# Optimization experiments

Hardware: AMD Instinct MI355X
Metric: run time of the kernel (lower is better)

The kernel has to match this reference:

```python
import jax, jax.numpy as jnp
import numpy as np
from jax import lax

EPS = 1e-8

def _conv(x, w, b):
    # x: [B,Cin,H,W], w: [Cout,Cin,kh,kw] (torch OIHW layout), SAME padding, stride 1
    y = lax.conv_general_dilated(x, w, (1, 1), 'SAME',
                                 dimension_numbers=('NCHW', 'OIHW', 'NCHW'))
    return y + b[None, :, None, None]

def setup_inputs() -> dict:
    key = jax.random.key(0)
    ks = jax.random.split(key, 16)
    B, S, H, A, NZ, NO = 256, 4, 32, 5, 150, 17
    d = {
        'map_in': jax.random.uniform(ks[0], (B, 2, H, H), jnp.float32),
        'b0': jax.random.uniform(ks[1], (B, H, H), jnp.float32),
        'act_in': jax.random.randint(ks[2], (B, S), 0, A),
        'obs_in': jax.random.uniform(ks[3], (B, S, 4), jnp.float32),
        'is_start': 1,
        'step_size': S,
        'VI_k': 64,
        # parameters, initialized per the torch init scheme
        'Tb_w': 1.0 / 9.0 + jax.random.normal(ks[4], (A, 1, 3, 3)) / 90.0,
        'Tb_b': jnp.zeros((A,)),
        'Tv_w': 1.0 / 9.0 + jax.random.normal(ks[5], (A, 1, 3, 3)) / 90.0,
        'Tv_b': jnp.zeros((A,)),
        'Z1_w': jax.random.normal(ks[6], (NZ, 1, 3, 3)) / 3.0,
        'Z1_b': jnp.zeros((NZ,)),
        'Z2_w': jax.random.normal(ks[7], (NO, NZ, 1, 1)) / np.sqrt(NZ),
        'Z2_b': jnp.zeros((NO,)),
        'O1_w': jax.random.normal(ks[8], (NO, 4)) * 0.25,
        'O1_b': jnp.zeros((NO,)),
        'O3_w': jax.random.normal(ks[9], (NO, NO)) / NO,
        'O3_b': jnp.zeros((NO,)),
        'R1_w': jax.random.normal(ks[10], (NZ, 2, 3, 3)) / np.sqrt(18.0),
        'R1_b': jnp.zeros((NZ,)),
        'R2_w': jax.random.normal(ks[11], (A, NZ, 1, 1)) / np.sqrt(NZ),
        'R2_b': jnp.zeros((A,)),
        'FL_w': jax.random.normal(ks[12], (A, A)) * 0.25,
        'FL_b': jnp.zeros((A,)),
    }
    return d

def reference(map_in, b0, act_in, obs_in, is_start, step_size, VI_k,
              Tb_w, Tb_b, Tv_w, Tv_b, Z1_w, Z1_b, Z2_w, Z2_b,
              O1_w, O1_b, O3_w, O3_b, R1_w, R1_b, R2_w, R2_b, FL_w, FL_b):
    B, _, H, W = map_in.shape
    A = Tb_w.shape[0]

    # ---- VI: value iteration conv+add+max loop ----
    R = _conv(jax.nn.relu(_conv(map_in, R1_w, R1_b)), R2_w, R2_b)  # [B,A,H,W]
    v0 = jnp.zeros((B, 1, H, W), map_in.dtype)
    Q0 = jnp.zeros_like(R)

    def vi_step(carry, _):
        v, _Q = carry
        Q = _conv(v, Tv_w, Tv_b) + R
        v = jnp.max(Q, axis=1, keepdims=True)
        return (v, Q), None

    (_, Q), _ = lax.scan(vi_step, (v0, Q0), None, length=VI_k)
    Q = jnp.transpose(Q, (0, 2, 3, 1))  # [B,H,W,A]

    # ---- observation model Z ----
    Z = jax.nn.sigmoid(_conv(_conv(map_in[:, :1], Z1_w, Z1_b), Z2_w, Z2_b))
    Z = jnp.transpose(Z, (0, 2, 3, 1))  # [B,H,W,17]
    Z = Z / (jnp.sum(Z, axis=3, keepdims=True) + EPS)

    # ---- recurrent Bayes filter + policy ----
    b = b0 if is_start else b0  # is_start resets belief to b0 (always true here)
    outs = []
    for t in range(step_size):  # small fixed recurrence length
        o = obs_in[:, t]  # [B,4]
        w = jax.nn.softmax(jnp.tanh(o @ O1_w.T + O1_b) @ O3_w.T + O3_b, axis=1)  # [B,17]
        Z_O = jnp.einsum('bhwo,bo->bhw', Z, w)
        bp = jnp.transpose(_conv(b[:, None], Tb_w, Tb_b), (0, 2, 3, 1))  # [B,H,W,A]
        a1h = jax.nn.one_hot(act_in[:, t], A, dtype=bp.dtype)
        b_pa = jnp.einsum('bhwa,ba->bhw', bp, a1h)
        b_next = b_pa * Z_O
        b = b_next / (jnp.sum(b_next, axis=(1, 2), keepdims=True) + EPS)
        Qb = jnp.einsum('bhwa,bhw->ba', Q, b)
        outs.append(Qb @ FL_w.T + FL_b)
    outputs = jnp.concatenate(outs, axis=0)  # [step_size*B, A]
    return outputs, b
```

## Files before the change

kernel.cpp:

```cpp
#include <hip/hip_runtime.h>

#define EPSV 1e-8f
#define PW   34
#define NPIX 1024
#define NA   5
#define NOUT 17
#define NZC  150
#define MAXS 8

__global__ __launch_bounds__(256) void k0_prep(
    const float* __restrict__ obs_in,
    const float* __restrict__ O1_w, const float* __restrict__ O1_b,
    const float* __restrict__ O3_w, const float* __restrict__ O3_b,
    const float* __restrict__ Z1_w, const float* __restrict__ Z1_b,
    const float* __restrict__ Z2_w, const float* __restrict__ Z2_b,
    float* __restrict__ w_all, float* __restrict__ zc, int S)
{
    __shared__ float h[MAXS*NOUT], u[MAXS*NOUT];
    const int tid = threadIdx.x, b = blockIdx.x;
    const int t = tid / NOUT, o = tid % NOUT;
    const bool act = (tid < S*NOUT);

    if (act) {
        const float* ob = obs_in + (b*S + t)*4;
        float hh = O1_b[o];
        #pragma unroll
        for (int k = 0; k < 4; ++k) hh += ob[k] * O1_w[o*4 + k];
        h[tid] = tanhf(hh);
    }
    __syncthreads();
    if (act) {
        float uu = O3_b[o];
        #pragma unroll
        for (int j = 0; j < NOUT; ++j) uu += h[t*NOUT + j] * O3_w[o*NOUT + j];
        u[tid] = uu;
    }
    __syncthreads();
    if (act) {
        float mx = u[t*NOUT];
        #pragma unroll
        for (int j = 1; j < NOUT; ++j) mx = fmaxf(mx, u[t*NOUT + j]);
        float sm = 0.f;
        #pragma unroll
        for (int j = 0; j < NOUT; ++j) sm += expf(u[t*NOUT + j] - mx);
        w_all[(b*MAXS + t)*NOUT + o] = expf(u[tid] - mx) / sm;
    }
    if (b == 0) {
        for (int j2 = tid; j2 < NOUT*9 + NOUT; j2 += 256) {
            if (j2 < NOUT*9) {
                const int oo = j2 / 9, k = j2 % 9;
                float s = 0.f;
                for (int c = 0; c < NZC; ++c) s += Z2_w[oo*NZC + c] * Z1_w[c*9 + k];
                zc[j2] = s;
            } else {
                const int oo = j2 - NOUT*9;
                float s = Z2_b[oo];
                for (int c = 0; c < NZC; ++c) s += Z2_w[oo*NZC + c] * Z1_b[c];
                zc[j2] = s;
            }
        }
    }
}

__global__ __launch_bounds__(256, 4) void k1_rz(
    const float* __restrict__ map_in,
    const float* __restrict__ R1_w, const float* __restrict__ R1_b,
    const float* __restrict__ R2_w, const float* __restrict__ R2_b,
    const float* __restrict__ w_all, const float* __restrict__ zc,
    float* __restrict__ r_out, float* __restrict__ zo_out, int S)
{
    __shared__ float t0[10*34], t1[10*34];
    const int tid = threadIdx.x;
    const int b = blockIdx.x >> 2, strip = blockIdx.x & 3;
    const int ty = tid >> 5, x = tid & 31;
    const int y = strip*8 + ty;
    const int pix = y*32 + x;

    for (int i = tid; i < 340; i += 256) {
        const int tr = i / 34, tc = i % 34;
        const int gy = strip*8 - 1 + tr, gx = tc - 1;
        const bool ok = (gy >= 0 && gy < 32 && gx >= 0 && gx < 32);
        t0[i] = ok ? map_in[b*2*NPIX + gy*32 + gx] : 0.f;
        t1[i] = ok ? map_in[b*2*NPIX + NPIX + gy*32 + gx] : 0.f;
    }
    __syncthreads();

    float m0[9], m1[9];
    #pragma unroll
    for (int k = 0; k < 9; ++k) {
        const int off = (ty + k/3)*34 + x + (k%3);
        m0[k] = t0[off]; m1[k] = t1[off];
    }

    float rA[NA], rB[NA];
    #pragma unroll
    for (int a = 0; a < NA; ++a) { rA[a] = R2_b[a]; rB[a] = 0.f; }
    for (int c = 0; c < NZC; c += 2) {
        const float* w1a = R1_w + c*18;
        const float* w1b = w1a + 18;
        float s0 = R1_b[c], s1 = R1_b[c+1];
        #pragma unroll
        for (int k = 0; k < 9; ++k) { s0 += m0[k] * w1a[k];   s1 += m0[k] * w1b[k]; }
        #pragma unroll
        for (int k = 0; k < 9; ++k) { s0 += m1[k] * w1a[9+k]; s1 += m1[k] * w1b[9+k]; }
        s0 = fmaxf(s0, 0.f); s1 = fmaxf(s1, 0.f);
        #pragma unroll
        for (int a = 0; a < NA; ++a) {
            rA[a] += R2_w[a*NZC + c]     * s0;
            rB[a] += R2_w[a*NZC + c + 1] * s1;
        }
    }
    #pragma unroll
    for (int a = 0; a < NA; ++a)
        r_out[(b*NA + a)*NPIX + pix] = rA[a] + rB[a];

    float z[NOUT];
    float zs = 0.f;
    #pragma unroll
    for (int o = 0; o < NOUT; ++o) {
        float s = zc[NOUT*9 + o];
        #pragma unroll
        for (int k = 0; k < 9; ++k) s += m0[k] * zc[o*9 + k];
        const float zz = 1.f / (1.f + expf(-s));
        z[o] = zz; zs += zz;
    }
    const float zn = 1.f / (zs + EPSV);
    for (int t = 0; t < S; ++t) {
        float zo = 0.f;
        #pragma unroll
        for (int o = 0; o < NOUT; ++o) zo += z[o] * w_all[(b*MAXS + t)*NOUT + o];
        zo_out[(b*S + t)*NPIX + pix] = zo * zn;
    }
}

__global__ __launch_bounds__(1024, 4) void k2_vib(
    const float* __restrict__ b0,   const int* __restrict__ act_in,
    const int*   __restrict__ step_p, const int* __restrict__ vik_p,
    const float* __restrict__ Tb_w, const float* __restrict__ Tb_b,
    const float* __restrict__ Tv_w, const float* __restrict__ Tv_b,
    const float* __restrict__ FL_w, const float* __restrict__ FL_b,
    const float* __restrict__ r_in, const float* __restrict__ zo_in,
    float* __restrict__ out, int B)
{
    __shared__ float v_lds[PW*PW], b_lds[PW*PW];
    __shared__ float partials[16][6], sums[6];

    const int tid  = threadIdx.x;
    const int blk  = blockIdx.x;
    const int y    = tid >> 5, x = tid & 31;
    const int pidx = (y + 1) * PW + (x + 1);
    const int lane = tid & 63, wvid = tid >> 6;

    const int S = step_p[0];
    const int K = vik_p[0];

    for (int i = tid; i < PW*PW; i += NPIX) { v_lds[i] = 0.f; b_lds[i] = 0.f; }
    __syncthreads();
    b_lds[pidx] = b0[blk*NPIX + tid];

    float r[NA];
    #pragma unroll
    for (int a = 0; a < NA; ++a)
        r[a] = r_in[(blk*NA + a)*NPIX + tid] + Tv_b[a];

    float q[NA];
    #pragma unroll
    for (int a = 0; a < NA; ++a) q[a] = 0.f;
    for (int it = 0; it < K; ++it) {
        float n[9];
        #pragma unroll
        for (int k = 0; k < 9; ++k) n[k] = v_lds[(y + k/3)*PW + x + (k%3)];
        float vmax = -3.4e38f;
        #pragma unroll
        for (int a = 0; a < NA; ++a) {
            float s = r[a];
            #pragma unroll
            for (int k = 0; k < 9; ++k) s += n[k] * Tv_w[a*9 + k];
            q[a] = s;
            vmax = fmaxf(vmax, s);
        }
        __syncthreads();
        v_lds[pidx] = vmax;
        __syncthreads();
    }

    for (int t = 0; t < S; ++t) {
        const int a_t = act_in[blk*S + t];
        float bp = Tb_b[a_t];
        #pragma unroll
        for (int k = 0; k < 9; ++k)
            bp += b_lds[(y + k/3)*PW + x + (k%3)] * Tb_w[a_t*9 + k];

        const float bn = bp * zo_in[(blk*S + t)*NPIX + tid];

        float v6[6];
        v6[5] = bn;
        #pragma unroll
        for (int a = 0; a < NA; ++a) v6[a] = q[a] * bn;
        #pragma unroll
        for (int k = 0; k < 6; ++k) {
            float vv = v6[k];
            for (int off = 32; off > 0; off >>= 1) vv += __shfl_down(vv, off);
            v6[k] = vv;
        }
        if (lane == 0) {
            #pragma unroll
            for (int k = 0; k < 6; ++k) partials[wvid][k] = v6[k];
        }
        __syncthreads();
        if (tid < 6) {
            float s = 0.f;
            for (int w2 = 0; w2 < 16; ++w2) s += partials[w2][tid];
            sums[tid] = s;
        }
        __syncthreads();

        const float inv = 1.f / (sums[5] + EPSV);
        if (tid < NA) {
            float oj = FL_b[tid];
            #pragma unroll
            for (int a = 0; a < NA; ++a) oj += (sums[a] * inv) * FL_w[tid*NA + a];
            out[(t*B + blk)*NA + tid] = oj;
        }
        b_lds[pidx] = bn * inv;
        __syncthreads();
    }

    out[S*B*NA + blk*NPIX + tid] = b_lds[pidx];
}

extern "C" void kernel_launch(void* const* d_in, const int* in_sizes, int n_in,
                              void* d_out, int out_size, void* d_ws, size_t ws_size,
                              hipStream_t stream)
{
    const float* map_in = (const float*)d_in[0];
    const float* b0     = (const float*)d_in[1];
    const int*   act_in = (const int*)  d_in[2];
    const float* obs_in = (const float*)d_in[3];
    const int*   step_p = (const int*)  d_in[5];
    const int*   vik_p  = (const int*)  d_in[6];
    const float* Tb_w = (const float*)d_in[7];
    const float* Tb_b = (const float*)d_in[8];
    const float* Tv_w = (const float*)d_in[9];
    const float* Tv_b = (const float*)d_in[10];
    const float* Z1_w = (const float*)d_in[11];
    const float* Z1_b = (const float*)d_in[12];
    const float* Z2_w = (const float*)d_in[13];
    const float* Z2_b = (const float*)d_in[14];
    const float* O1_w = (const float*)d_in[15];
    const float* O1_b = (const float*)d_in[16];
    const float* O3_w = (const float*)d_in[17];
    const float* O3_b = (const float*)d_in[18];
    const float* R1_w = (const float*)d_in[19];
    const float* R1_b = (const float*)d_in[20];
    const float* R2_w = (const float*)d_in[21];
    const float* R2_b = (const float*)d_in[22];
    const float* FL_w = (const float*)d_in[23];
    const float* FL_b = (const float*)d_in[24];

    const int B = in_sizes[1] / NPIX;
    const int S = in_sizes[2] / B;

    float* ws    = (float*)d_ws;
    float* w_all = ws;
    float* zc    = w_all + (size_t)B*MAXS*NOUT;
    float* r_ws  = zc + 192;
    float* zo_ws = r_ws + (size_t)B*NA*NPIX;

    hipLaunchKernelGGL(k0_prep, dim3(B), dim3(256), 0, stream,
        obs_in, O1_w, O1_b, O3_w, O3_b, Z1_w, Z1_b, Z2_w, Z2_b, w_all, zc, S);

    hipLaunchKernelGGL(k1_rz, dim3(B*4), dim3(256), 0, stream,
        map_in, R1_w, R1_b, R2_w, R2_b, w_all, zc, r_ws, zo_ws, S);

    hipLaunchKernelGGL(k2_vib, dim3(B), dim3(1024), 0, stream,
        b0, act_in, step_p, vik_p, Tb_w, Tb_b, Tv_w, Tv_b, FL_w, FL_b,
        r_ws, zo_ws, (float*)d_out, B);
}
```

Baseline: 214.1 us.

## Split R-conv channel reduction across two thread groups with partial sums

k1_rz now assigns 128 pixels per block and splits the 150 hidden channels into two halves, one per 128-thread group. Each group writes its partial reward sums to a doubled workspace, and k2_vib adds the two partials when loading r. This doubles the grid and shortens the serial per-thread channel loop to expose more parallelism. The cost is extra global traffic for the partials, a Z computation that leaves half the threads idle, and a larger workspace.

```diff
diff --git a/kernel.cpp b/kernel.cpp
--- a/kernel.cpp
+++ b/kernel.cpp
@@ -6,6 +6,7 @@
 #define NA   5
 #define NOUT 17
 #define NZC  150
+#define NZH  75
 #define MAXS 8
 
 __global__ __launch_bounds__(256) void k0_prep(
@@ -62,26 +63,29 @@
     }
 }
 
-__global__ __launch_bounds__(256, 4) void k1_rz(
+__global__ __launch_bounds__(256, 8) void k1_rz(
     const float* __restrict__ map_in,
     const float* __restrict__ R1_w, const float* __restrict__ R1_b,
     const float* __restrict__ R2_w, const float* __restrict__ R2_b,
     const float* __restrict__ w_all, const float* __restrict__ zc,
-    float* __restrict__ r_out, float* __restrict__ zo_out, int S)
-{
-    __shared__ float t0[10*34], t1[10*34];
+    float* __restrict__ r_part, float* __restrict__ zo_out, int S)
+{
+    __shared__ float t0[6*34], t1[6*34];
     const int tid = threadIdx.x;
-    const int b = blockIdx.x >> 2, strip = blockIdx.x & 3;
-    const int ty = tid >> 5, x = tid & 31;
-    const int y = strip*8 + ty;
+    const int b = blockIdx.x >> 3, strip = blockIdx.x & 7;
+    const int p  = tid & 127;
+    const int cg = tid >> 7;
+    const int ty = p >> 5, x = p & 31;
+    const int y = strip*4 + ty;
     const int pix = y*32 + x;
 
-    for (int i = tid; i < 340; i += 256) {
-        const int tr = i / 34, tc = i % 34;
-        const int gy = strip*8 - 1 + tr, gx = tc - 1;
+    for (int i = tid; i < 2*204; i += 256) {
+        const int ch = i / 204, j = i % 204;
+        const int tr = j / 34, tc = j % 34;
+        const int gy = strip*4 - 1 + tr, gx = tc - 1;
         const bool ok = (gy >= 0 && gy < 32 && gx >= 0 && gx < 32);
-        t0[i] = ok ? map_in[b*2*NPIX + gy*32 + gx] : 0.f;
-        t1[i] = ok ? map_in[b*2*NPIX + NPIX + gy*32 + gx] : 0.f;
+        const float v = ok ? map_in[b*2*NPIX + ch*NPIX + gy*32 + gx] : 0.f;
+        if (ch == 0) t0[j] = v; else t1[j] = v;
     }
     __syncthreads();
 
@@ -92,44 +96,43 @@
         m0[k] = t0[off]; m1[k] = t1[off];
     }
 
-    float rA[NA], rB[NA];
-    #pragma unroll
-    for (int a = 0; a < NA; ++a) { rA[a] = R2_b[a]; rB[a] = 0.f; }
-    for (int c = 0; c < NZC; c += 2) {
-        const float* w1a = R1_w + c*18;
-        const float* w1b = w1a + 18;
-        float s0 = R1_b[c], s1 = R1_b[c+1];
-        #pragma unroll
-        for (int k = 0; k < 9; ++k) { s0 += m0[k] * w1a[k];   s1 += m0[k] * w1b[k]; }
-        #pragma unroll
-        for (int k = 0; k < 9; ++k) { s0 += m1[k] * w1a[9+k]; s1 += m1[k] * w1b[9+k]; }
-        s0 = fmaxf(s0, 0.f); s1 = fmaxf(s1, 0.f);
-        #pragma unroll
-        for (int a = 0; a < NA; ++a) {
-            rA[a] += R2_w[a*NZC + c]     * s0;
-            rB[a] += R2_w[a*NZC + c + 1] * s1;
-        }
+    float r[NA];
+    #pragma unroll
+    for (int a = 0; a < NA; ++a) r[a] = (cg == 0) ? R2_b[a] : 0.f;
+    const int c0 = cg * NZH;
+    for (int c = c0; c < c0 + NZH; ++c) {
+        float s = R1_b[c];
+        const float* w1 = R1_w + c*18;
+        #pragma unroll
+        for (int k = 0; k < 9; ++k) s += m0[k] * w1[k];
+        #pragma unroll
+        for (int k = 0; k < 9; ++k) s += m1[k] * w1[9 + k];
+        s = fmaxf(s, 0.f);
+        #pragma unroll
+        for (int a = 0; a < NA; ++a) r[a] += R2_w[a*NZC + c] * s;
     }
     #pragma unroll
     for (int a = 0; a < NA; ++a)
-        r_out[(b*NA + a)*NPIX + pix] = rA[a] + rB[a];
-
-    float z[NOUT];
-    float zs = 0.f;
-    #pragma unroll
-    for (int o = 0; o < NOUT; ++o) {
-        float s = zc[NOUT*9 + o];
-        #pragma unroll
-        for (int k = 0; k < 9; ++k) s += m0[k] * zc[o*9 + k];
-        const float zz = 1.f / (1.f + expf(-s));
-        z[o] = zz; zs += zz;
-    }
-    const float zn = 1.f / (zs + EPSV);
-    for (int t = 0; t < S; ++t) {
-        float zo = 0.f;
-        #pragma unroll
-        for (int o = 0; o < NOUT; ++o) zo += z[o] * w_all[(b*MAXS + t)*NOUT + o];
-        zo_out[(b*S + t)*NPIX + pix] = zo * zn;
+        r_part[(((size_t)b*2 + cg)*NA + a)*NPIX + pix] = r[a];
+
+    if (cg == 0) {
+        float z[NOUT];
+        float zs = 0.f;
+        #pragma unroll
+        for (int o = 0; o < NOUT; ++o) {
+            float s = zc[NOUT*9 + o];
+            #pragma unroll
+            for (int k = 0; k < 9; ++k) s += m0[k] * zc[o*9 + k];
+            const float zz = 1.f / (1.f + expf(-s));
+            z[o] = zz; zs += zz;
+        }
+        const float zn = 1.f / (zs + EPSV);
+        for (int t = 0; t < S; ++t) {
+            float zo = 0.f;
+            #pragma unroll
+            for (int o = 0; o < NOUT; ++o) zo += z[o] * w_all[(b*MAXS + t)*NOUT + o];
+            zo_out[((size_t)b*S + t)*NPIX + pix] = zo * zn;
+        }
     }
 }
 
@@ -139,7 +142,7 @@
     const float* __restrict__ Tb_w, const float* __restrict__ Tb_b,
     const float* __restrict__ Tv_w, const float* __restrict__ Tv_b,
     const float* __restrict__ FL_w, const float* __restrict__ FL_b,
-    const float* __restrict__ r_in, const float* __restrict__ zo_in,
+    const float* __restrict__ r_part, const float* __restrict__ zo_in,
     float* __restrict__ out, int B)
 {
     __shared__ float v_lds[PW*PW], b_lds[PW*PW];
@@ -161,7 +164,9 @@
     float r[NA];
     #pragma unroll
     for (int a = 0; a < NA; ++a)
-        r[a] = r_in[(blk*NA + a)*NPIX + tid] + Tv_b[a];
+        r[a] = r_part[(((size_t)blk*2 + 0)*NA + a)*NPIX + tid]
+             + r_part[(((size_t)blk*2 + 1)*NA + a)*NPIX + tid]
+             + Tv_b[a];
 
     float q[NA];
     #pragma unroll
@@ -191,7 +196,7 @@
         for (int k = 0; k < 9; ++k)
             bp += b_lds[(y + k/3)*PW + x + (k%3)] * Tb_w[a_t*9 + k];
 
-        const float bn = bp * zo_in[(blk*S + t)*NPIX + tid];
+        const float bn = bp * zo_in[((size_t)blk*S + t)*NPIX + tid];
 
         float v6[6];
         v6[5] = bn;
@@ -265,12 +270,12 @@
     float* w_all = ws;
     float* zc    = w_all + (size_t)B*MAXS*NOUT;
     float* r_ws  = zc + 192;
-    float* zo_ws = r_ws + (size_t)B*NA*NPIX;
+    float* zo_ws = r_ws + (size_t)B*2*NA*NPIX;
 
     hipLaunchKernelGGL(k0_prep, dim3(B), dim3(256), 0, stream,
         obs_in, O1_w, O1_b, O3_w, O3_b, Z1_w, Z1_b, Z2_w, Z2_b, w_all, zc, S);
 
-    hipLaunchKernelGGL(k1_rz, dim3(B*4), dim3(256), 0, stream,
+    hipLaunchKernelGGL(k1_rz, dim3(B*8), dim3(256), 0, stream,
         map_in, R1_w, R1_b, R2_w, R2_b, w_all, zc, r_ws, zo_ws, S);
 
     hipLaunchKernelGGL(k2_vib, dim3(B), dim3(1024), 0, stream,
```

New measurement: 272.2 us. +27.1%, slower.
